# Kernel optimization log

Measured on AMD Instinct MI355X. Metric: run time of the kernel, lower is better.

## Reference

```python
import jax, jax.numpy as jnp
import numpy as np

B, F, D = 4096, 39, 16          # batch, num_field, embedding_size
V = 1000000                     # num_feat (vocab)
H1, H2 = 128, 128               # cin_layer_sizes
INPUT_DIM = F * D               # 624
FC_DIM = H1 // 2 + H2           # 192 (split_half)
DEEP = [400, 400]
BN_EPS = 1e-5


def setup_inputs() -> dict:
    key = jax.random.key(0)
    ks = jax.random.split(key, 16)
    xav = lambda k, shp: jax.random.normal(k, shp, jnp.float32) * np.sqrt(2.0 / (shp[0] + shp[-1]))
    return {
        "feat_index": jax.random.randint(ks[0], (B, F), 0, V),
        "feat_value": jax.random.uniform(ks[1], (B, F), jnp.float32),
        "emb_table": xav(ks[2], (V, D)),
        "linear_w": xav(ks[3], (INPUT_DIM, 1)),
        "linear_b": jnp.zeros((1,), jnp.float32),
        "conv_w1": xav(ks[4], (H1, F, F)),          # (out, h_prev, m) == conv1d 1x1 weight reshaped
        "conv_b1": jnp.zeros((H1,), jnp.float32),
        "conv_w2": xav(ks[5], (H2, H1 // 2, F)),
        "conv_b2": jnp.zeros((H2,), jnp.float32),
        "deep_w1": xav(ks[6], (INPUT_DIM, DEEP[0])),
        "deep_b1": jnp.zeros((DEEP[0],), jnp.float32),
        "bn_g1": jnp.ones((DEEP[0],), jnp.float32),
        "bn_b1": jnp.zeros((DEEP[0],), jnp.float32),
        "deep_w2": xav(ks[7], (DEEP[0], DEEP[1])),
        "deep_b2": jnp.zeros((DEEP[1],), jnp.float32),
        "bn_g2": jnp.ones((DEEP[1],), jnp.float32),
        "bn_b2": jnpp if False else jnp.zeros((DEEP[1],), jnp.float32),
        "out_w": xav(ks[8], (1 + FC_DIM + DEEP[1], 1)),
        "out_b": jnp.zeros((1,), jnp.float32),
    }


def _bn(x, g, b):
    # torch BatchNorm1d in training mode: biased batch variance
    m = x.mean(axis=0)
    v = x.var(axis=0)
    return g * (x - m) * jax.lax.rsqrt(v + BN_EPS) + b


def reference(feat_index, feat_value, emb_table, linear_w, linear_b,
              conv_w1, conv_b1, conv_w2, conv_b2,
              deep_w1, deep_b1, bn_g1, bn_b1,
              deep_w2, deep_b2, bn_g2, bn_b2,
              out_w, out_b):
    e = emb_table[feat_index]                      # [B, F, D]
    flat = e.reshape(e.shape[0], -1)               # [B, F*D]
    linear_part = flat @ linear_w + linear_b       # [B, 1]

    # CIN: fused outer-product + 1x1 conv (x_k[b,o,d] = sum_{h,m} W[o,h,m] x_prev[b,h,d] x0[b,m,d])
    x0 = e
    h1 = jax.nn.relu(jnp.einsum('bhd,bmd,ohm->bod', x0, x0, conv_w1) + conv_b1[None, :, None])
    nxt, hi1 = jnp.split(h1, 2, axis=1)            # split_half
    h2 = jax.nn.relu(jnp.einsum('bhd,bmd,ohm->bod', nxt, x0, conv_w2) + conv_b2[None, :, None])
    res = jnp.concatenate([hi1, h2], axis=1).sum(axis=2)   # [B, FC_DIM]

    # Deep tower (dropout off / deterministic)
    y = jax.nn.relu(_bn(flat @ deep_w1 + deep_b1, bn_g1, bn_b1))
    y = jax.nn.relu(_bn(y @ deep_w2 + deep_b2, bn_g2, bn_b2))

    cat = jnp.concatenate([linear_part, res, y], axis=1)   # [B, 593]
    return cat @ out_w + out_b
```

## Files before the change

kernel.cpp:

```cpp
#include <hip/hip_runtime.h>

#define BATCH   4096
#define NF      39
#define ED      16
#define IN_DIM  624
#define DW      400
#define BN_EPS  1e-5f
#define AK1     640
#define NKS1    20
#define NKS2    13
#define WCOL    416
#define NK1     117
#define NK2     156

typedef __attribute__((ext_vector_type(8))) short short8;
typedef __attribute__((ext_vector_type(16))) float f32x16;
typedef __attribute__((ext_vector_type(4))) float f32x4;
typedef __attribute__((ext_vector_type(2))) float f32x2;
typedef unsigned short u16;

__device__ inline unsigned pack_hi2(float a, float b) {
  return __builtin_amdgcn_perm(__float_as_uint(b), __float_as_uint(a), 0x07060302u);
}
__device__ inline unsigned bf16_rne(float f) {
  unsigned u = __float_as_uint(f);
  u += 0x7fff + ((u >> 16) & 1);
  return u >> 16;
}
__device__ inline float bf2f(u16 v) { return __uint_as_float((unsigned)v << 16); }

#define CIN1_E (NK1 * 2048)
#define CIN2_E (NK2 * 2048)
#define D1_E  (NKS1 * WCOL * 32)
#define D2_E  (NKS2 * WCOL * 32)
#define PREP_E (CIN1_E + CIN2_E + D1_E + D2_E + 1600)
#define PREP_B ((PREP_E + 255) / 256)
#define GATH_B (BATCH / 4)

__global__ __launch_bounds__(256) void k_gp(const int* __restrict__ idx,
    const float* __restrict__ emb, const float* __restrict__ lw,
    const float* __restrict__ lb, const float* __restrict__ w1,
    const float* __restrict__ w2, const float* __restrict__ dw1,
    const float* __restrict__ dw2, u16* __restrict__ flatb,
    float* __restrict__ lp, u16* __restrict__ wp1, u16* __restrict__ wp2,
    u16* __restrict__ wpd1, u16* __restrict__ wpd2, float* __restrict__ gstat) {
  int t = threadIdx.x;
  if (blockIdx.x < GATH_B) {
    int lane = t & 63;
    int b = blockIdx.x * 4 + (t >> 6);
    int sj = (lane < NF) ? idx[b * NF + lane] : 0;
    float acc = 0.f;
#pragma unroll
    for (int i = 0; i < 10; i++) {
      int e = lane + i * 64;
      if (e < IN_DIM) {
        int f = e >> 4;
        int row = __shfl(sj, f);
        float v = emb[(size_t)row * ED + (e & 15)];
        flatb[(size_t)b * AK1 + e] = (u16)bf16_rne(v);
        acc = fmaf(v, lw[e], acc);
      } else {
        flatb[(size_t)b * AK1 + e] = 0;
      }
    }
#pragma unroll
    for (int k = 1; k < 64; k <<= 1) acc += __shfl_xor(acc, k);
    if (lane == 0) lp[b] = acc + lb[0];
  } else {
    int e = (blockIdx.x - GATH_B) * 256 + t;
    if (e < CIN1_E) {
      int k16 = e >> 11, r = e & 2047, col = r >> 4, kk = r & 15;
      int mg = k16 / 3, sg = k16 - mg * 3;
      int h = sg * 16 + kk;
      wp1[e] = (h < NF) ? (u16)bf16_rne(w1[(size_t)col * (NF * NF) + h * NF + mg])
                        : (u16)0;
    } else if (e < CIN1_E + CIN2_E) {
      int e2 = e - CIN1_E;
      int k16 = e2 >> 11, r = e2 & 2047, col = r >> 4, kk = r & 15;
      int k = k16 * 16 + kk, h = k & 63, m = k >> 6;
      wp2[e2] = (u16)bf16_rne(w2[(size_t)col * (64 * NF) + h * NF + m]);
    } else if (e < CIN1_E + CIN2_E + D1_E) {
      int e2 = e - CIN1_E - CIN2_E;
      int ksg = e2 / (WCOL * 32), r = e2 - ksg * (WCOL * 32);
      int col = r >> 5, kk = r & 31;
      int k = ksg * 32 + kk;
      wpd1[e2] = (k < IN_DIM && col < DW) ? (u16)bf16_rne(dw1[(size_t)k * DW + col]) : 0;
    } else if (e < CIN1_E + CIN2_E + D1_E + D2_E) {
      int e2 = e - CIN1_E - CIN2_E - D1_E;
      int ksg = e2 / (WCOL * 32), r = e2 - ksg * (WCOL * 32);
      int col = r >> 5, kk = r & 31;
      int k = ksg * 32 + kk;
      wpd2[e2] = (k < DW && col < DW) ? (u16)bf16_rne(dw2[(size_t)k * DW + col]) : 0;
    } else if (e < PREP_E) {
      gstat[e - CIN1_E - CIN2_E - D1_E - D2_E] = 0.f;
    }
  }
}

__global__ __launch_bounds__(256, 4) void k_cin_f(
    const u16* __restrict__ flatb, const u16* __restrict__ wp1,
    const u16* __restrict__ wp2, const float* __restrict__ bias1,
    const float* __restrict__ bias2, float* __restrict__ res) {
  __shared__ __align__(16) u16 s1b[4 * 16 * 64];
  int t = threadIdx.x;
  int ow = t >> 6, lane = t & 63;
  int col = lane & 31, khalf = lane >> 5;
  int si = (lane >> 4) & 1, d = lane & 15;
  int b0 = blockIdx.x * 4;
  const u16* fb = flatb + (size_t)(b0 + si) * AK1;

  f32x16 acc[2];
#pragma unroll
  for (int p = 0; p < 2; p++)
#pragma unroll
    for (int r = 0; r < 16; r++) acc[p][r] = 0.f;

  const u16* wb1 = wp1 + (size_t)(ow * 32 + col) * 16 + khalf * 8;

#pragma unroll 1
  for (int sq = 0; sq < 3; sq++) {
    f32x2 sp1[2][4];
#pragma unroll
    for (int p = 0; p < 2; p++)
#pragma unroll
      for (int w4 = 0; w4 < 4; w4++) {
        int h0 = sq * 16 + khalf * 8 + 2 * w4;
        int h1 = h0 + 1;
        float f0 = (h0 < NF) ? bf2f(fb[p * 1280 + h0 * 16 + d]) : 0.f;
        float f1 = (h1 < NF) ? bf2f(fb[p * 1280 + h1 * 16 + d]) : 0.f;
        sp1[p][w4] = (f32x2){f0, f1};
      }

    const u16* wbs = wb1 + (size_t)sq * 2048;
    short8 bfr[3];
    bfr[0] = *(const short8*)(wbs);
    bfr[1] = *(const short8*)(wbs + (size_t)3 * 2048);
    float xvr[3][2];
    xvr[0][0] = bf2f(fb[d]);       xvr[0][1] = bf2f(fb[1280 + d]);
    xvr[1][0] = bf2f(fb[16 + d]);  xvr[1][1] = bf2f(fb[1280 + 16 + d]);

#pragma unroll 1
    for (int mg = 0; mg < 13; mg++) {
#pragma unroll
      for (int jm = 0; jm < 3; jm++) {
        int m = mg * 3 + jm;
        int mn = m + 2; mn = (mn > 39) ? 39 : mn;
        xvr[(jm + 2) % 3][0] = bf2f(fb[mn * 16 + d]);
        xvr[(jm + 2) % 3][1] = bf2f(fb[1280 + mn * 16 + d]);
        bfr[(jm + 2) % 3] = *(const short8*)(wbs + (size_t)(m + 2) * 3 * 2048);
        __builtin_amdgcn_s_setprio(1);
#pragma unroll
        for (int p = 0; p < 2; p++) {
          union { unsigned u[4]; short8 v; } a;
          f32x2 xv2 = (f32x2){xvr[jm][p], xvr[jm][p]};
#pragma unroll
          for (int w4 = 0; w4 < 4; w4++) {
            f32x2 pr = sp1[p][w4] * xv2;
            a.u[w4] = pack_hi2(pr[0], pr[1]);
          }
          acc[p] = __builtin_amdgcn_mfma_f32_32x32x16_bf16(
              a.v, bfr[jm], acc[p], 0, 0, 0);
        }
        __builtin_amdgcn_s_setprio(0);
      }
    }
  }

  if (ow < 2) {
#pragma unroll
    for (int p = 0; p < 2; p++) {
      int o = ow * 32 + col;
      float bi = bias1[o];
#pragma unroll
      for (int r = 0; r < 16; r++) {
        int smp = p * 2 + (r >> 3);
        int dd = (r & 3) + 8 * ((r >> 2) & 1) + 4 * khalf;
        float v = fmaxf(acc[p][r] + bi, 0.f);
        int ix = (((smp * 16 + dd) * 64) + o) ^ ((dd & 7) << 3);
        s1b[ix] = (u16)bf16_rne(v);
      }
    }
  } else {
#pragma unroll
    for (int p = 0; p < 2; p++) {
      int o = ow * 32 + col;
      float bi = bias1[o];
      float p0 = 0.f, p1 = 0.f;
#pragma unroll
      for (int r = 0; r < 8; r++)  p0 += fmaxf(acc[p][r] + bi, 0.f);
#pragma unroll
      for (int r = 8; r < 16; r++) p1 += fmaxf(acc[p][r] + bi, 0.f);
      p0 += __shfl_xor(p0, 32);
      p1 += __shfl_xor(p1, 32);
      if (khalf == 0) {
        res[(size_t)(b0 + p * 2) * 192 + (o - 64)] = p0;
        res[(size_t)(b0 + p * 2 + 1) * 192 + (o - 64)] = p1;
      }
    }
  }

  __syncthreads();

#pragma unroll
  for (int p = 0; p < 2; p++)
#pragma unroll
    for (int r = 0; r < 16; r++) acc[p][r] = 0.f;

  const u16* wb2 = wp2 + (size_t)(ow * 32 + col) * 16 + khalf * 8;

#pragma unroll 1
  for (int sq = 0; sq < 4; sq++) {
    f32x2 sp2[2][4];
#pragma unroll
    for (int p = 0; p < 2; p++) {
      int smp = p * 2 + si;
      int ix = ((smp * 16 + d) * 64 + sq * 16 + khalf * 8) ^ ((d & 7) << 3);
      union { short8 v; u16 e[8]; } vv;
      vv.v = *(const short8*)(s1b + ix);
#pragma unroll
      for (int w4 = 0; w4 < 4; w4++)
        sp2[p][w4] = (f32x2){bf2f(vv.e[2 * w4]), bf2f(vv.e[2 * w4 + 1])};
    }

    const u16* wbs = wb2 + (size_t)sq * 2048;
    short8 bq[3];
    bq[0] = *(const short8*)(wbs);
    bq[1] = *(const short8*)(wbs + (size_t)4 * 2048);
    float xvr[3][2];
    xvr[0][0] = bf2f(fb[d]);       xvr[0][1] = bf2f(fb[1280 + d]);
    xvr[1][0] = bf2f(fb[16 + d]);  xvr[1][1] = bf2f(fb[1280 + 16 + d]);

#pragma unroll 1
    for (int mg = 0; mg < 13; mg++) {
#pragma unroll
      for (int jm = 0; jm < 3; jm++) {
        int m = mg * 3 + jm;
        int mn = m + 2; mn = (mn > 39) ? 39 : mn;
        xvr[(jm + 2) % 3][0] = bf2f(fb[mn * 16 + d]);
        xvr[(jm + 2) % 3][1] = bf2f(fb[1280 + mn * 16 + d]);
        bq[(jm + 2) % 3] = *(const short8*)(wbs + (size_t)(m + 2) * 4 * 2048);
        __builtin_amdgcn_s_setprio(1);
#pragma unroll
        for (int p = 0; p < 2; p++) {
          union { unsigned u[4]; short8 v; } a;
          f32x2 xv2 = (f32x2){xvr[jm][p], xvr[jm][p]};
#pragma unroll
          for (int w4 = 0; w4 < 4; w4++) {
            f32x2 pr = sp2[p][w4] * xv2;
            a.u[w4] = pack_hi2(pr[0], pr[1]);
          }
          acc[p] = __builtin_amdgcn_mfma_f32_32x32x16_bf16(
              a.v, bq[jm], acc[p], 0, 0, 0);
        }
        __builtin_amdgcn_s_setprio(0);
      }
    }
  }

#pragma unroll
  for (int p = 0; p < 2; p++) {
    int o = ow * 32 + col;
    float bi = bias2[o];
    float p0 = 0.f, p1 = 0.f;
#pragma unroll
    for (int r = 0; r < 8; r++)  p0 += fmaxf(acc[p][r] + bi, 0.f);
#pragma unroll
    for (int r = 8; r < 16; r++) p1 += fmaxf(acc[p][r] + bi, 0.f);
    p0 += __shfl_xor(p0, 32);
    p1 += __shfl_xor(p1, 32);
    if (khalf == 0) {
      res[(size_t)(b0 + p * 2) * 192 + 64 + o] = p0;
      res[(size_t)(b0 + p * 2 + 1) * 192 + 64 + o] = p1;
    }
  }
}

template <bool BN_A, int NKS, int KREAL, int AK>
__global__ __launch_bounds__(256) void k_gemm_mfma(
    const u16* __restrict__ Abf, const float* __restrict__ Af32,
    const u16* __restrict__ wp, const float* __restrict__ bias,
    const float* __restrict__ gsIn, const float* __restrict__ gs2In,
    const float* __restrict__ bng, const float* __restrict__ bnb,
    float* __restrict__ C, float* __restrict__ gs, float* __restrict__ gs2) {
  __shared__ float lsS[NKS * 32], lsH[NKS * 32];
  __shared__ float lred[64];
  int t = threadIdx.x;
  if (BN_A) {
    for (int c = t; c < NKS * 32; c += 256) {
      float sc = 0.f, sh = 0.f;
      if (c < DW) {
        float m = gsIn[c] * (1.f / BATCH);
        float var = gs2In[c] * (1.f / BATCH) - m * m;
        sc = bng[c] * rsqrtf(var + BN_EPS);
        sh = bnb[c] - m * sc;
      }
      lsS[c] = sc; lsH[c] = sh;
    }
  }
  if (t < 64) lred[t] = 0.f;
  __syncthreads();

  int w = t >> 6, lane = t & 63;
  int nl = lane & 15, q = lane >> 4;
  int row = blockIdx.x * 64 + w * 16 + nl;
  int c0 = blockIdx.y * 32;
  f32x4 acc[2];
  acc[0] = (f32x4){0.f, 0.f, 0.f, 0.f};
  acc[1] = (f32x4){0.f, 0.f, 0.f, 0.f};

  short8 araw[2]; f32x4 fraw0[2], fraw1[2]; short8 braw[2][2];
  auto loadA_raw = [&](int ksg, int buf) {
    int kb = ksg * 32 + q * 8;
    if (!BN_A) {
      araw[buf] = *(const short8*)(Abf + (size_t)row * AK + kb);
    } else {
      if (kb + 8 <= KREAL) {
        fraw0[buf] = *(const f32x4*)(Af32 + (size_t)row * KREAL + kb);
        fraw1[buf] = *(const f32x4*)(Af32 + (size_t)row * KREAL + kb + 4);
      } else {
        fraw0[buf] = (f32x4){0.f,0.f,0.f,0.f};
        fraw1[buf] = (f32x4){0.f,0.f,0.f,0.f};
      }
    }
    const u16* wb = wp + (size_t)ksg * (WCOL * 32) + (size_t)(c0 + nl) * 32 + q * 8;
    braw[buf][0] = *(const short8*)wb;
    braw[buf][1] = *(const short8*)(wb + 16 * 32);
  };
  auto cookA = [&](int ksg, int buf) -> short8 {
    if (!BN_A) return araw[buf];
    int kb = ksg * 32 + q * 8;
    f32x4 s0 = *(const f32x4*)&lsS[kb], h0 = *(const f32x4*)&lsH[kb];
    f32x4 s1 = *(const f32x4*)&lsS[kb + 4], h1 = *(const f32x4*)&lsH[kb + 4];
    union { unsigned u[4]; short8 s; } a;
    float v0 = fmaxf(fmaf(fraw0[buf][0], s0[0], h0[0]), 0.f);
    float v1 = fmaxf(fmaf(fraw0[buf][1], s0[1], h0[1]), 0.f);
    float v2 = fmaxf(fmaf(fraw0[buf][2], s0[2], h0[2]), 0.f);
    float v3 = fmaxf(fmaf(fraw0[buf][3], s0[3], h0[3]), 0.f);
    float v4 = fmaxf(fmaf(fraw1[buf][0], s1[0], h1[0]), 0.f);
    float v5 = fmaxf(fmaf(fraw1[buf][1], s1[1], h1[1]), 0.f);
    float v6 = fmaxf(fmaf(fraw1[buf][2], s1[2], h1[2]), 0.f);
    float v7 = fmaxf(fmaf(fraw1[buf][3], s1[3], h1[3]), 0.f);
    a.u[0] = bf16_rne(v0) | (bf16_rne(v1) << 16);
    a.u[1] = bf16_rne(v2) | (bf16_rne(v3) << 16);
    a.u[2] = bf16_rne(v4) | (bf16_rne(v5) << 16);
    a.u[3] = bf16_rne(v6) | (bf16_rne(v7) << 16);
    return a.s;
  };

  loadA_raw(0, 0);
#pragma unroll 4
  for (int ksg = 0; ksg < NKS; ksg++) {
    int cur = ksg & 1;
    if (ksg + 1 < NKS) loadA_raw(ksg + 1, cur ^ 1);
    short8 afr = cookA(ksg, cur);
    acc[0] = __builtin_amdgcn_mfma_f32_16x16x32_bf16(afr, braw[cur][0], acc[0], 0, 0, 0);
    acc[1] = __builtin_amdgcn_mfma_f32_16x16x32_bf16(afr, braw[cur][1], acc[1], 0, 0, 0);
  }

  int rbase = blockIdx.x * 64 + w * 16 + q * 4;
#pragma unroll
  for (int nt = 0; nt < 2; nt++) {
    int col = c0 + nt * 16 + nl;
    if (col < DW) {
      float bi = bias[col];
      float s = 0.f, s2 = 0.f;
#pragma unroll
      for (int r = 0; r < 4; r++) {
        float v = acc[nt][r] + bi;
        C[(size_t)(rbase + r) * DW + col] = v;
        s += v; s2 = fmaf(v, v, s2);
      }
      s += __shfl_xor(s, 16); s2 += __shfl_xor(s2, 16);
      s += __shfl_xor(s, 32); s2 += __shfl_xor(s2, 32);
      if (q == 0) {
        atomicAdd(&lred[nt * 16 + nl], s);
        atomicAdd(&lred[32 + nt * 16 + nl], s2);
      }
    }
  }
  __syncthreads();
  if (t < 32) {
    int col = c0 + t;
    if (col < DW) atomicAdd(&gs[col], lred[t]);
  } else if (t < 64) {
    int col = c0 + t - 32;
    if (col < DW) atomicAdd(&gs2[col], lred[t]);
  }
}

__global__ __launch_bounds__(256) void k_final(const float* __restrict__ lp,
    const float* __restrict__ res, const float* __restrict__ y2,
    const float* __restrict__ gB, const float* __restrict__ gB2,
    const float* __restrict__ g2, const float* __restrict__ bb2,
    const float* __restrict__ ow, const float* __restrict__ ob,
    float* __restrict__ out) {
  __shared__ float lsS[DW], lsH[DW];
  int t = threadIdx.x;
  for (int c = t; c < DW; c += 256) {
    float m = gB[c] * (1.f / BATCH);
    float var = gB2[c] * (1.f / BATCH) - m * m;
    float sc = g2[c] * rsqrtf(var + BN_EPS);
    lsS[c] = sc;
    lsH[c] = bb2[c] - m * sc;
  }
  __syncthreads();
  int lane = t & 63, w = t >> 6;
  int b = blockIdx.x * 4 + w;
  float acc = 0.f;
  for (int j = lane; j < 593; j += 64) {
    float v;
    if (j == 0)       v = lp[b];
    else if (j < 193) v = res[(size_t)b * 192 + (j - 1)];
    else {
      int c = j - 193;
      v = fmaxf(fmaf(y2[(size_t)b * DW + c], lsS[c], lsH[c]), 0.f);
    }
    acc = fmaf(v, ow[j], acc);
  }
#pragma unroll
  for (int k = 1; k < 64; k <<= 1) acc += __shfl_xor(acc, k);
  if (lane == 0) out[b] = acc + ob[0];
}

extern "C" void kernel_launch(void* const* d_in, const int* in_sizes, int n_in,
                              void* d_out, int out_size, void* d_ws, size_t ws_size,
                              hipStream_t stream) {
  const int*   feat_index = (const int*)d_in[0];
  const float* emb = (const float*)d_in[2];
  const float* lw  = (const float*)d_in[3];
  const float* lb  = (const float*)d_in[4];
  const float* w1  = (const float*)d_in[5];
  const float* b1  = (const float*)d_in[6];
  const float* w2  = (const float*)d_in[7];
  const float* b2  = (const float*)d_in[8];
  const float* dw1 = (const float*)d_in[9];
  const float* db1 = (const float*)d_in[10];
  const float* g1  = (const float*)d_in[11];
  const float* bb1 = (const float*)d_in[12];
  const float* dw2 = (const float*)d_in[13];
  const float* db2 = (const float*)d_in[14];
  const float* g2  = (const float*)d_in[15];
  const float* bb2 = (const float*)d_in[16];
  const float* ow  = (const float*)d_in[17];
  const float* ob  = (const float*)d_in[18];

  float* ws   = (float*)d_ws;
  u16*  flatb = (u16*)ws;
  float* y1   = ws + 1310720;
  float* res  = ws + 2949120;
  float* lp   = ws + 3735552;
  float* gA   = ws + 3741248;
  float* gA2  = gA + 400;
  float* gB   = gA2 + 400;
  float* gB2  = gB + 400;
  float* y2   = ws + 3742848;
  u16*  wp1   = (u16*)(ws + 5381248);
  u16*  wp2   = (u16*)(ws + 5501056);
  u16*  wpd1  = (u16*)(ws + 5660800);
  u16*  wpd2  = (u16*)(ws + 5793920);
  float* out  = (float*)d_out;

  k_gp<<<GATH_B + PREP_B, 256, 0, stream>>>(feat_index, emb, lw, lb, w1, w2,
      dw1, dw2, flatb, lp, wp1, wp2, wpd1, wpd2, gA);
  k_cin_f<<<1024, 256, 0, stream>>>(flatb, wp1, wp2, b1, b2, res);
  k_gemm_mfma<false, NKS1, IN_DIM, AK1><<<dim3(BATCH / 64, 13), 256, 0, stream>>>(
      flatb, nullptr, wpd1, db1, nullptr, nullptr, nullptr, nullptr, y1, gA, gA2);
  k_gemm_mfma<true, NKS2, DW, 0><<<dim3(BATCH / 64, 13), 256, 0, stream>>>(
      nullptr, y1, wpd2, db2, gA, gA2, g1, bb1, y2, gB, gB2);
  k_final<<<BATCH / 4, 256, 0, stream>>>(lp, res, y2, gB, gB2, g2, bb2, ow, ob, out);
}
```

Baseline: 265.7 us.

## Split CIN kernel K-range across waves with 2x2 MFMA tiles and LDS reduction

Each wave of the fused CIN kernel now covers 64 output channels (two 32-wide N tiles) over half of the m range, instead of 32 channels over the full range. Every A fragment built from the outer product therefore feeds two MFMAs, which halves the VALU multiply and pack work per MFMA. The two K-halves are summed through a new 32KB LDS exchange buffer before the bias/ReLU epilogues. This adds accumulator registers, LDS traffic and an extra barrier, and drops the occupancy hint of 4 blocks per CU.

```diff
diff --git a/kernel.cpp b/kernel.cpp
--- a/kernel.cpp
+++ b/kernel.cpp
@@ -97,120 +97,166 @@
   }
 }
 
-__global__ __launch_bounds__(256, 4) void k_cin_f(
+__global__ __launch_bounds__(256) void k_cin_f(
     const u16* __restrict__ flatb, const u16* __restrict__ wp1,
     const u16* __restrict__ wp2, const float* __restrict__ bias1,
     const float* __restrict__ bias2, float* __restrict__ res) {
+  __shared__ __align__(16) float exch[4][32][64];
   __shared__ __align__(16) u16 s1b[4 * 16 * 64];
   int t = threadIdx.x;
-  int ow = t >> 6, lane = t & 63;
+  int w = t >> 6, lane = t & 63;
+  int oh = w & 1, kh = w >> 1;
   int col = lane & 31, khalf = lane >> 5;
   int si = (lane >> 4) & 1, d = lane & 15;
   int b0 = blockIdx.x * 4;
-  const u16* fb = flatb + (size_t)(b0 + si) * AK1;
-
-  f32x16 acc[2];
+  const u16* fb  = flatb + (size_t)(b0 + si) * AK1;
+  const u16* fbm = fb + kh * 20 * 16;
+
+  f32x16 acc[2][2];
 #pragma unroll
   for (int p = 0; p < 2; p++)
 #pragma unroll
-    for (int r = 0; r < 16; r++) acc[p][r] = 0.f;
-
-  const u16* wb1 = wp1 + (size_t)(ow * 32 + col) * 16 + khalf * 8;
-
+    for (int nt = 0; nt < 2; nt++)
+#pragma unroll
+      for (int r = 0; r < 16; r++) acc[p][nt][r] = 0.f;
+
+  const u16* wb1 = wp1 + (size_t)(oh * 64 + col) * 16 + khalf * 8
+                       + (size_t)kh * 20 * 3 * 2048;
 #pragma unroll 1
   for (int sq = 0; sq < 3; sq++) {
-    f32x2 sp1[2][4];
+    f32x2 sp[2][4];
 #pragma unroll
     for (int p = 0; p < 2; p++)
 #pragma unroll
       for (int w4 = 0; w4 < 4; w4++) {
-        int h0 = sq * 16 + khalf * 8 + 2 * w4;
-        int h1 = h0 + 1;
+        int h0 = sq * 16 + khalf * 8 + 2 * w4, h1 = h0 + 1;
         float f0 = (h0 < NF) ? bf2f(fb[p * 1280 + h0 * 16 + d]) : 0.f;
         float f1 = (h1 < NF) ? bf2f(fb[p * 1280 + h1 * 16 + d]) : 0.f;
-        sp1[p][w4] = (f32x2){f0, f1};
-      }
-
+        sp[p][w4] = (f32x2){f0, f1};
+      }
     const u16* wbs = wb1 + (size_t)sq * 2048;
-    short8 bfr[3];
-    bfr[0] = *(const short8*)(wbs);
-    bfr[1] = *(const short8*)(wbs + (size_t)3 * 2048);
-    float xvr[3][2];
-    xvr[0][0] = bf2f(fb[d]);       xvr[0][1] = bf2f(fb[1280 + d]);
-    xvr[1][0] = bf2f(fb[16 + d]);  xvr[1][1] = bf2f(fb[1280 + 16 + d]);
-
-#pragma unroll 1
-    for (int mg = 0; mg < 13; mg++) {
-#pragma unroll
-      for (int jm = 0; jm < 3; jm++) {
-        int m = mg * 3 + jm;
-        int mn = m + 2; mn = (mn > 39) ? 39 : mn;
-        xvr[(jm + 2) % 3][0] = bf2f(fb[mn * 16 + d]);
-        xvr[(jm + 2) % 3][1] = bf2f(fb[1280 + mn * 16 + d]);
-        bfr[(jm + 2) % 3] = *(const short8*)(wbs + (size_t)(m + 2) * 3 * 2048);
-        __builtin_amdgcn_s_setprio(1);
-#pragma unroll
-        for (int p = 0; p < 2; p++) {
-          union { unsigned u[4]; short8 v; } a;
-          f32x2 xv2 = (f32x2){xvr[jm][p], xvr[jm][p]};
-#pragma unroll
-          for (int w4 = 0; w4 < 4; w4++) {
-            f32x2 pr = sp1[p][w4] * xv2;
-            a.u[w4] = pack_hi2(pr[0], pr[1]);
-          }
-          acc[p] = __builtin_amdgcn_mfma_f32_32x32x16_bf16(
-              a.v, bfr[jm], acc[p], 0, 0, 0);
+    short8 bc0 = *(const short8*)(wbs);
+    short8 bc1 = *(const short8*)(wbs + 512);
+    float xc0 = bf2f(fbm[d]), xc1 = bf2f(fbm[1280 + d]);
+#pragma unroll
+    for (int mj = 0; mj < 20; mj++) {
+      short8 bn0 = *(const short8*)(wbs + (size_t)(mj + 1) * 6144);
+      short8 bn1 = *(const short8*)(wbs + (size_t)(mj + 1) * 6144 + 512);
+      float xn0 = bf2f(fbm[(mj + 1) * 16 + d]);
+      float xn1 = bf2f(fbm[1280 + (mj + 1) * 16 + d]);
+      __builtin_amdgcn_s_setprio(1);
+      {
+        union { unsigned u[4]; short8 v; } a;
+        f32x2 xv2 = (f32x2){xc0, xc0};
+#pragma unroll
+        for (int w4 = 0; w4 < 4; w4++) {
+          f32x2 pr = sp[0][w4] * xv2;
+          a.u[w4] = pack_hi2(pr[0], pr[1]);
         }
-        __builtin_amdgcn_s_setprio(0);
-      }
-    }
-  }
-
-  if (ow < 2) {
-#pragma unroll
-    for (int p = 0; p < 2; p++) {
-      int o = ow * 32 + col;
-      float bi = bias1[o];
-#pragma unroll
-      for (int r = 0; r < 16; r++) {
-        int smp = p * 2 + (r >> 3);
-        int dd = (r & 3) + 8 * ((r >> 2) & 1) + 4 * khalf;
-        float v = fmaxf(acc[p][r] + bi, 0.f);
-        int ix = (((smp * 16 + dd) * 64) + o) ^ ((dd & 7) << 3);
-        s1b[ix] = (u16)bf16_rne(v);
-      }
-    }
-  } else {
-#pragma unroll
-    for (int p = 0; p < 2; p++) {
-      int o = ow * 32 + col;
-      float bi = bias1[o];
-      float p0 = 0.f, p1 = 0.f;
-#pragma unroll
-      for (int r = 0; r < 8; r++)  p0 += fmaxf(acc[p][r] + bi, 0.f);
-#pragma unroll
-      for (int r = 8; r < 16; r++) p1 += fmaxf(acc[p][r] + bi, 0.f);
-      p0 += __shfl_xor(p0, 32);
-      p1 += __shfl_xor(p1, 32);
+        acc[0][0] = __builtin_amdgcn_mfma_f32_32x32x16_bf16(a.v, bc0, acc[0][0], 0, 0, 0);
+        acc[0][1] = __builtin_amdgcn_mfma_f32_32x32x16_bf16(a.v, bc1, acc[0][1], 0, 0, 0);
+      }
+      {
+        union { unsigned u[4]; short8 v; } a;
+        f32x2 xv2 = (f32x2){xc1, xc1};
+#pragma unroll
+        for (int w4 = 0; w4 < 4; w4++) {
+          f32x2 pr = sp[1][w4] * xv2;
+          a.u[w4] = pack_hi2(pr[0], pr[1]);
+        }
+        acc[1][0] = __builtin_amdgcn_mfma_f32_32x32x16_bf16(a.v, bc0, acc[1][0], 0, 0, 0);
+        acc[1][1] = __builtin_amdgcn_mfma_f32_32x32x16_bf16(a.v, bc1, acc[1][1], 0, 0, 0);
+      }
+      __builtin_amdgcn_s_setprio(0);
+      bc0 = bn0; bc1 = bn1; xc0 = xn0; xc1 = xn1;
+    }
+  }
+
+  auto xstore = [&](const f32x16 (&A)[2], int slot) {
+#pragma unroll
+    for (int nt = 0; nt < 2; nt++)
+#pragma unroll
+      for (int r = 0; r < 16; r++)
+        exch[slot][nt * 16 + r][lane] = A[nt][r];
+  };
+  auto xadd = [&](f32x16 (&A)[2], int slot) {
+#pragma unroll
+    for (int nt = 0; nt < 2; nt++)
+#pragma unroll
+      for (int r = 0; r < 16; r++)
+        A[nt][r] += exch[slot][nt * 16 + r][lane];
+  };
+  auto epi1 = [&](const f32x16 (&A)[2], int P) {
+    if (oh == 0) {
+#pragma unroll
+      for (int nt = 0; nt < 2; nt++) {
+        int o = nt * 32 + col;
+        float bi = bias1[o];
+#pragma unroll
+        for (int r = 0; r < 16; r++) {
+          int smp = P * 2 + (r >> 3);
+          int dd = (r & 3) + 8 * ((r >> 2) & 1) + 4 * khalf;
+          float v = fmaxf(A[nt][r] + bi, 0.f);
+          int ix = (((smp * 16 + dd) * 64) + o) ^ ((dd & 7) << 3);
+          s1b[ix] = (u16)bf16_rne(v);
+        }
+      }
+    } else {
+#pragma unroll
+      for (int nt = 0; nt < 2; nt++) {
+        int o = 64 + nt * 32 + col;
+        float bi = bias1[o];
+        float q0 = 0.f, q1 = 0.f;
+#pragma unroll
+        for (int r = 0; r < 8; r++)  q0 += fmaxf(A[nt][r] + bi, 0.f);
+#pragma unroll
+        for (int r = 8; r < 16; r++) q1 += fmaxf(A[nt][r] + bi, 0.f);
+        q0 += __shfl_xor(q0, 32);
+        q1 += __shfl_xor(q1, 32);
+        if (khalf == 0) {
+          res[(size_t)(b0 + P * 2) * 192 + (o - 64)] = q0;
+          res[(size_t)(b0 + P * 2 + 1) * 192 + (o - 64)] = q1;
+        }
+      }
+    }
+  };
+  auto epi2 = [&](const f32x16 (&A)[2], int P) {
+#pragma unroll
+    for (int nt = 0; nt < 2; nt++) {
+      int o = oh * 64 + nt * 32 + col;
+      float bi = bias2[o];
+      float q0 = 0.f, q1 = 0.f;
+#pragma unroll
+      for (int r = 0; r < 8; r++)  q0 += fmaxf(A[nt][r] + bi, 0.f);
+#pragma unroll
+      for (int r = 8; r < 16; r++) q1 += fmaxf(A[nt][r] + bi, 0.f);
+      q0 += __shfl_xor(q0, 32);
+      q1 += __shfl_xor(q1, 32);
       if (khalf == 0) {
-        res[(size_t)(b0 + p * 2) * 192 + (o - 64)] = p0;
-        res[(size_t)(b0 + p * 2 + 1) * 192 + (o - 64)] = p1;
-      }
-    }
-  }
-
+        res[(size_t)(b0 + P * 2) * 192 + 64 + o] = q0;
+        res[(size_t)(b0 + P * 2 + 1) * 192 + 64 + o] = q1;
+      }
+    }
+  };
+
+  if (kh == 0) xstore(acc[1], oh * 2 + 1); else xstore(acc[0], oh * 2);
   __syncthreads();
+  if (kh == 0) { xadd(acc[0], oh * 2);     epi1(acc[0], 0); }
+  else         { xadd(acc[1], oh * 2 + 1); epi1(acc[1], 1); }
+  __syncthreads();
 
 #pragma unroll
   for (int p = 0; p < 2; p++)
 #pragma unroll
-    for (int r = 0; r < 16; r++) acc[p][r] = 0.f;
-
-  const u16* wb2 = wp2 + (size_t)(ow * 32 + col) * 16 + khalf * 8;
-
+    for (int nt = 0; nt < 2; nt++)
+#pragma unroll
+      for (int r = 0; r < 16; r++) acc[p][nt][r] = 0.f;
+
+  const u16* wb2 = wp2 + (size_t)(oh * 64 + col) * 16 + khalf * 8
+                       + (size_t)kh * 20 * 4 * 2048;
 #pragma unroll 1
   for (int sq = 0; sq < 4; sq++) {
-    f32x2 sp2[2][4];
+    f32x2 sp[2][4];
 #pragma unroll
     for (int p = 0; p < 2; p++) {
       int smp = p * 2 + si;
@@ -219,60 +265,50 @@
       vv.v = *(const short8*)(s1b + ix);
 #pragma unroll
       for (int w4 = 0; w4 < 4; w4++)
-        sp2[p][w4] = (f32x2){bf2f(vv.e[2 * w4]), bf2f(vv.e[2 * w4 + 1])};
-    }
-
+        sp[p][w4] = (f32x2){bf2f(vv.e[2 * w4]), bf2f(vv.e[2 * w4 + 1])};
+    }
     const u16* wbs = wb2 + (size_t)sq * 2048;
-    short8 bq[3];
-    bq[0] = *(const short8*)(wbs);
-    bq[1] = *(const short8*)(wbs + (size_t)4 * 2048);
-    float xvr[3][2];
-    xvr[0][0] = bf2f(fb[d]);       xvr[0][1] = bf2f(fb[1280 + d]);
-    xvr[1][0] = bf2f(fb[16 + d]);  xvr[1][1] = bf2f(fb[1280 + 16 + d]);
-
-#pragma unroll 1
-    for (int mg = 0; mg < 13; mg++) {
-#pragma unroll
-      for (int jm = 0; jm < 3; jm++) {
-        int m = mg * 3 + jm;
-        int mn = m + 2; mn = (mn > 39) ? 39 : mn;
-        xvr[(jm + 2) % 3][0] = bf2f(fb[mn * 16 + d]);
-        xvr[(jm + 2) % 3][1] = bf2f(fb[1280 + mn * 16 + d]);
-        bq[(jm + 2) % 3] = *(const short8*)(wbs + (size_t)(m + 2) * 4 * 2048);
-        __builtin_amdgcn_s_setprio(1);
-#pragma unroll
-        for (int p = 0; p < 2; p++) {
-          union { unsigned u[4]; short8 v; } a;
-          f32x2 xv2 = (f32x2){xvr[jm][p], xvr[jm][p]};
-#pragma unroll
-          for (int w4 = 0; w4 < 4; w4++) {
-            f32x2 pr = sp2[p][w4] * xv2;
-            a.u[w4] = pack_hi2(pr[0], pr[1]);
-          }
-          acc[p] = __builtin_amdgcn_mfma_f32_32x32x16_bf16(
-              a.v, bq[jm], acc[p], 0, 0, 0);
+    short8 bc0 = *(const short8*)(wbs);
+    short8 bc1 = *(const short8*)(wbs + 512);
+    float xc0 = bf2f(fbm[d]), xc1 = bf2f(fbm[1280 + d]);
+#pragma unroll
+    for (int mj = 0; mj < 20; mj++) {
+      short8 bn0 = *(const short8*)(wbs + (size_t)(mj + 1) * 8192);
+      short8 bn1 = *(const short8*)(wbs + (size_t)(mj + 1) * 8192 + 512);
+      float xn0 = bf2f(fbm[(mj + 1) * 16 + d]);
+      float xn1 = bf2f(fbm[1280 + (mj + 1) * 16 + d]);
+      __builtin_amdgcn_s_setprio(1);
+      {
+        union { unsigned u[4]; short8 v; } a;
+        f32x2 xv2 = (f32x2){xc0, xc0};
+#pragma unroll
+        for (int w4 = 0; w4 < 4; w4++) {
+          f32x2 pr = sp[0][w4] * xv2;
+          a.u[w4] = pack_hi2(pr[0], pr[1]);
         }
-        __builtin_amdgcn_s_setprio(0);
-      }
-    }
-  }
-
-#pragma unroll
-  for (int p = 0; p < 2; p++) {
-    int o = ow * 32 + col;
-    float bi = bias2[o];
-    float p0 = 0.f, p1 = 0.f;
-#pragma unroll
-    for (int r = 0; r < 8; r++)  p0 += fmaxf(acc[p][r] + bi, 0.f);
-#pragma unroll
-    for (int r = 8; r < 16; r++) p1 += fmaxf(acc[p][r] + bi, 0.f);
-    p0 += __shfl_xor(p0, 32);
-    p1 += __shfl_xor(p1, 32);
-    if (khalf == 0) {
-      res[(size_t)(b0 + p * 2) * 192 + 64 + o] = p0;
-      res[(size_t)(b0 + p * 2 + 1) * 192 + 64 + o] = p1;
-    }
-  }
+        acc[0][0] = __builtin_amdgcn_mfma_f32_32x32x16_bf16(a.v, bc0, acc[0][0], 0, 0, 0);
+        acc[0][1] = __builtin_amdgcn_mfma_f32_32x32x16_bf16(a.v, bc1, acc[0][1], 0, 0, 0);
+      }
+      {
+        union { unsigned u[4]; short8 v; } a;
+        f32x2 xv2 = (f32x2){xc1, xc1};
+#pragma unroll
+        for (int w4 = 0; w4 < 4; w4++) {
+          f32x2 pr = sp[1][w4] * xv2;
+          a.u[w4] = pack_hi2(pr[0], pr[1]);
+        }
+        acc[1][0] = __builtin_amdgcn_mfma_f32_32x32x16_bf16(a.v, bc0, acc[1][0], 0, 0, 0);
+        acc[1][1] = __builtin_amdgcn_mfma_f32_32x32x16_bf16(a.v, bc1, acc[1][1], 0, 0, 0);
+      }
+      __builtin_amdgcn_s_setprio(0);
+      bc0 = bn0; bc1 = bn1; xc0 = xn0; xc1 = xn1;
+    }
+  }
+
+  if (kh == 0) xstore(acc[1], oh * 2 + 1); else xstore(acc[0], oh * 2);
+  __syncthreads();
+  if (kh == 0) { xadd(acc[0], oh * 2);     epi2(acc[0], 0); }
+  else         { xadd(acc[1], oh * 2 + 1); epi2(acc[1], 1); }
 }
 
 template <bool BN_A, int NKS, int KREAL, int AK>
```

After: 268.9 us. Within noise of the previous version (+1.2%).
